# Kernel tuning notes

Hardware: AMD Instinct MI355X
Metric: run time of the kernel (lower is better)

Reference implementation:

```python
import jax, jax.numpy as jnp
import numpy as np

# DeepSeek-V3 MLA attention (q_lora_rank > 0 path), sdpa attn_type (causal)
B, S, DIM = 2, 2048, 2048
NH = 16
Q_LORA = 1536
KV_LORA = 512
NOPE = 128
ROPE = 64
VH = 128
QK_HD = NOPE + ROPE  # 192
EPS = 1e-6
SCALE = QK_HD ** -0.5
ROPE_THETA = 10000.0


def _freqs(seqlen, dim, base):
    f = 1.0 / base ** (np.arange(0, dim, 2, dtype=np.float32) / dim)
    ang = np.outer(np.arange(seqlen, dtype=np.float32), f)
    return jnp.asarray(np.cos(ang)), jnp.asarray(np.sin(ang))


def rmsnorm(x, w, eps=EPS):
    var = jnp.mean(jnp.square(x), axis=-1, keepdims=True)
    return x * jax.lax.rsqrt(var + eps) * w


def apply_rope(x, cos, sin):
    # x: [b, s, h, d]; cos/sin: [s, d//2]; interleaved complex pairs (x[2i], x[2i+1])
    xr, xi = x[..., 0::2], x[..., 1::2]
    c = cos[None, :, None, :]
    s = sin[None, :, None, :]
    yr = xr * c - xi * s
    yi = xr * s + xi * c
    return jnp.stack([yr, yi], axis=-1).reshape(x.shape)


def setup_inputs() -> dict:
    key = jax.random.key(0)
    ks = jax.random.split(key, 7)
    std = 0.02
    x = jax.random.normal(ks[0], (B, S, DIM), dtype=jnp.float32)
    cos, sin = _freqs(S, ROPE, ROPE_THETA)
    return {
        "x": x,
        "freqs_cos": cos,
        "freqs_sin": sin,
        "wq_a": jax.random.normal(ks[1], (DIM, Q_LORA), dtype=jnp.float32) * std,
        "q_norm_w": jnp.ones((Q_LORA,), dtype=jnp.float32),
        "wq_b": jax.random.normal(ks[2], (Q_LORA, NH * QK_HD), dtype=jnp.float32) * std,
        "wkv_a": jax.random.normal(ks[3], (DIM, KV_LORA + ROPE), dtype=jnp.float32) * std,
        "kv_norm_w": jnp.ones((KV_LORA,), dtype=jnp.float32),
        "wkv_b": jax.random.normal(ks[4], (KV_LORA, NH * (NOPE + VH)), dtype=jnp.float32) * std,
        "wo": jax.random.normal(ks[5], (NH * VH, DIM), dtype=jnp.float32) * std,
    }


def reference(x, freqs_cos, freqs_sin, wq_a, q_norm_w, wq_b, wkv_a, kv_norm_w, wkv_b, wo):
    b, s, _ = x.shape
    # low-rank Q projection: wq_a -> RMSNorm -> wq_b
    q = rmsnorm(x @ wq_a, q_norm_w) @ wq_b
    q = q.reshape(b, s, NH, QK_HD)
    q_nope, q_pe = q[..., :NOPE], q[..., NOPE:]
    q_pe = apply_rope(q_pe, freqs_cos, freqs_sin)
    q = jnp.concatenate([q_nope, q_pe], axis=-1)
    # low-rank KV: wkv_a -> split latent / rope part
    kv = x @ wkv_a
    kv_lat, k_pe = kv[..., :KV_LORA], kv[..., KV_LORA:]
    k_pe = apply_rope(k_pe[:, :, None, :], freqs_cos, freqs_sin)  # [b,s,1,ROPE]
    kv = rmsnorm(kv_lat, kv_norm_w) @ wkv_b
    kv = kv.reshape(b, s, NH, NOPE + VH)
    k_nope, v = kv[..., :NOPE], kv[..., NOPE:]
    k = jnp.concatenate([k_nope, jnp.broadcast_to(k_pe, (b, s, NH, ROPE))], axis=-1)
    # attention [b,h,s,d]
    q = q.transpose(0, 2, 1, 3)
    k = k.transpose(0, 2, 1, 3)
    v = v.transpose(0, 2, 1, 3)
    scores = jnp.einsum("bhqd,bhkd->bhqk", q, k) * SCALE
    causal = jnp.tril(jnp.ones((s, s), dtype=bool))
    scores = jnp.where(causal[None, None], scores, jnp.finfo(scores.dtype).min)
    probs = jax.nn.softmax(scores, axis=-1)
    out = jnp.einsum("bhqk,bhkd->bhqd", probs, v)
    out = out.transpose(0, 2, 1, 3).reshape(b, s, NH * VH)
    return out @ wo
```

## Files before the change

kernel.cpp:

```cpp
#include <hip/hip_runtime.h>
#include <cstdint>
#include <cstddef>

typedef __attribute__((ext_vector_type(8))) short bf16x8;
typedef __attribute__((ext_vector_type(4))) float f32x4;
typedef __attribute__((ext_vector_type(16))) float f32x16;

#define S_LEN 2048
#define SCALE2 0.10411754f

__device__ __forceinline__ ushort f2bf(float f) {
  uint32_t u = __float_as_uint(f);
  u = (u + 0x7FFFu + ((u >> 16) & 1u)) >> 16;
  return (ushort)u;
}
__device__ __forceinline__ float bf2f(ushort u) {
  return __uint_as_float(((uint32_t)u) << 16);
}

typedef __attribute__((address_space(1))) void GV;
typedef __attribute__((address_space(3))) void LV;
__device__ __forceinline__ void gload16(const void* g, void* l) {
  __builtin_amdgcn_global_load_lds((GV*)g, (LV*)l, 16, 0, 0);
}

__device__ __forceinline__ void store_out(float* p, float v) { *p = v; }
__device__ __forceinline__ void store_out(ushort* p, float v) { *p = f2bf(v); }

__global__ void k_f32_to_bf16(const float* __restrict__ in, ushort* __restrict__ out, int n4) {
  int i = blockIdx.x * blockDim.x + threadIdx.x;
  int stride = gridDim.x * blockDim.x;
  for (; i < n4; i += stride) {
    float4 v = reinterpret_cast<const float4*>(in)[i];
    ushort4 o;
    o.x = f2bf(v.x); o.y = f2bf(v.y); o.z = f2bf(v.z); o.w = f2bf(v.w);
    reinterpret_cast<ushort4*>(out)[i] = o;
  }
}

__global__ void k_transpose_f32_bf16(const float* __restrict__ in, ushort* __restrict__ out,
                                     int R, int C) {
  __shared__ float tile[32][33];
  int c0 = blockIdx.x * 32, r0 = blockIdx.y * 32;
  int tx = threadIdx.x, ty = threadIdx.y;
#pragma unroll
  for (int i = 0; i < 32; i += 8) {
    int r = r0 + ty + i, c = c0 + tx;
    if (r < R && c < C) tile[ty + i][tx] = in[(size_t)r * C + c];
  }
  __syncthreads();
#pragma unroll
  for (int i = 0; i < 32; i += 8) {
    int c = c0 + ty + i, r = r0 + tx;
    if (r < R && c < C) out[(size_t)c * R + r] = f2bf(tile[tx][ty + i]);
  }
}

template <typename OUT>
__global__ __launch_bounds__(256) void k_gemm(const ushort* __restrict__ A,
                                              const ushort* __restrict__ Bt,
                                              OUT* __restrict__ C, int K, int Nreal) {
  __shared__ ushort As[128 * 72];
  __shared__ ushort Bs[128 * 72];
  const int t = threadIdx.x, lane = t & 63, w = t >> 6;
  const int nwg = gridDim.x * gridDim.y;
  const int wg = blockIdx.y * gridDim.x + blockIdx.x;
  const int swz = (wg & 7) * (nwg >> 3) + (wg >> 3);
  const int m0 = (swz / gridDim.x) * 128, n0 = (swz % gridDim.x) * 128;
  const int wm = (w >> 1) * 64, wn = (w & 1) * 64;
  const int g = lane >> 4, q = lane & 15;
  f32x4 acc[4][4] = {};
  for (int kt = 0; kt < K; kt += 64) {
#pragma unroll
    for (int it = 0; it < 5; ++it) {
      int ii = it * 4 + w;
      if (ii < 18) {
        unsigned s = ii * 64 + lane;
        int r = s / 9, e = s - r * 9;
        int cg = e ^ ((r >> 3) & 7);
        if (cg > 7) cg = 0;
        gload16(A + (size_t)(m0 + r) * K + kt + cg * 8, (char*)As + ii * 1024);
        gload16(Bt + (size_t)(n0 + r) * K + kt + cg * 8, (char*)Bs + ii * 1024);
      }
    }
    asm volatile("s_waitcnt vmcnt(0)" ::: "memory");
    __syncthreads();
#pragma unroll
    for (int kh = 0; kh < 2; ++kh) {
      bf16x8 af[4], bfr[4];
#pragma unroll
      for (int mi = 0; mi < 4; mi++) {
        int row = wm + 16 * mi + q;
        int rx = (row >> 3) & 7;
        af[mi] = *(const bf16x8*)(As + row * 72 + (((kh * 4 + g) ^ rx) << 3));
      }
#pragma unroll
      for (int ni = 0; ni < 4; ni++) {
        int row = wn + 16 * ni + q;
        int rx = (row >> 3) & 7;
        bfr[ni] = *(const bf16x8*)(Bs + row * 72 + (((kh * 4 + g) ^ rx) << 3));
      }
#pragma unroll
      for (int mi = 0; mi < 4; mi++)
#pragma unroll
        for (int ni = 0; ni < 4; ni++)
          acc[mi][ni] = __builtin_amdgcn_mfma_f32_16x16x32_bf16(af[mi], bfr[ni], acc[mi][ni], 0, 0, 0);
    }
    __syncthreads();
  }
#pragma unroll
  for (int mi = 0; mi < 4; mi++)
#pragma unroll
    for (int ni = 0; ni < 4; ni++) {
      int col = n0 + wn + 16 * ni + q;
      if (col < Nreal) {
        int row = m0 + wm + 16 * mi + 4 * g;
#pragma unroll
        for (int r = 0; r < 4; r++)
          store_out(&C[(size_t)(row + r) * Nreal + col], acc[mi][ni][r]);
      }
    }
}

__global__ __launch_bounds__(256) void k_gemm_kv(const ushort* __restrict__ A,
                                                 const ushort* __restrict__ Bt,
                                                 ushort* __restrict__ kbuf,
                                                 ushort* __restrict__ vT, int K) {
  __shared__ ushort As[128 * 72];
  __shared__ ushort Bs[128 * 72];
  const int t = threadIdx.x, lane = t & 63, w = t >> 6;
  const int nwg = gridDim.x * gridDim.y;
  const int wg = blockIdx.y * gridDim.x + blockIdx.x;
  const int swz = (wg & 7) * (nwg >> 3) + (wg >> 3);
  const int m0 = (swz / gridDim.x) * 128, n0 = (swz % gridDim.x) * 128;
  const int wm = (w >> 1) * 64, wn = (w & 1) * 64;
  const int g = lane >> 4, q = lane & 15;
  f32x4 acc[4][4] = {};
  for (int kt = 0; kt < K; kt += 64) {
#pragma unroll
    for (int it = 0; it < 5; ++it) {
      int ii = it * 4 + w;
      if (ii < 18) {
        unsigned s = ii * 64 + lane;
        int r = s / 9, e = s - r * 9;
        int cg = e ^ ((r >> 3) & 7);
        if (cg > 7) cg = 0;
        gload16(A + (size_t)(m0 + r) * K + kt + cg * 8, (char*)As + ii * 1024);
        gload16(Bt + (size_t)(n0 + r) * K + kt + cg * 8, (char*)Bs + ii * 1024);
      }
    }
    asm volatile("s_waitcnt vmcnt(0)" ::: "memory");
    __syncthreads();
#pragma unroll
    for (int kh = 0; kh < 2; ++kh) {
      bf16x8 af[4], bfr[4];
#pragma unroll
      for (int mi = 0; mi < 4; mi++) {
        int row = wm + 16 * mi + q;
        int rx = (row >> 3) & 7;
        af[mi] = *(const bf16x8*)(As + row * 72 + (((kh * 4 + g) ^ rx) << 3));
      }
#pragma unroll
      for (int ni = 0; ni < 4; ni++) {
        int row = wn + 16 * ni + q;
        int rx = (row >> 3) & 7;
        bfr[ni] = *(const bf16x8*)(Bs + row * 72 + (((kh * 4 + g) ^ rx) << 3));
      }
#pragma unroll
      for (int mi = 0; mi < 4; mi++)
#pragma unroll
        for (int ni = 0; ni < 4; ni++)
          acc[mi][ni] = __builtin_amdgcn_mfma_f32_16x16x32_bf16(af[mi], bfr[ni], acc[mi][ni], 0, 0, 0);
    }
    __syncthreads();
  }
#pragma unroll
  for (int mi = 0; mi < 4; mi++)
#pragma unroll
    for (int ni = 0; ni < 4; ni++) {
      int col = n0 + wn + 16 * ni + q;
      int hh = col >> 8, jj = col & 255;
      int row0 = m0 + wm + 16 * mi + 4 * g;
#pragma unroll
      for (int r = 0; r < 4; r++) {
        int tok = row0 + r;
        int bb = tok >> 11, ss = tok & 2047;
        ushort v = f2bf(acc[mi][ni][r]);
        if (jj < 128)
          kbuf[((size_t)(bb * 16 + hh) * 2048 + ss) * 192 + jj] = v;
        else
          vT[((size_t)(bb * 16 + hh) * 128 + (jj - 128)) * 2048 + ss] = v;
      }
    }
}

__global__ void k_rmsnorm_bf16(const float* __restrict__ in, const float* __restrict__ w,
                               ushort* __restrict__ out, int D, int instride) {
  int row = blockIdx.x;
  const float* x = in + (size_t)row * instride;
  ushort* o = out + (size_t)row * D;
  float ss = 0.f;
  for (int i = threadIdx.x; i < D; i += 256) { float v = x[i]; ss += v * v; }
#pragma unroll
  for (int m = 1; m < 64; m <<= 1) ss += __shfl_xor(ss, m);
  __shared__ float red[4];
  if ((threadIdx.x & 63) == 0) red[threadIdx.x >> 6] = ss;
  __syncthreads();
  float tot = red[0] + red[1] + red[2] + red[3];
  float sc = rsqrtf(tot / (float)D + 1e-6f);
  for (int i = threadIdx.x; i < D; i += 256) o[i] = f2bf(x[i] * sc * w[i]);
}

__global__ void k_kvnorm_rope(const float* __restrict__ cqkv, const float* __restrict__ w,
                              const float* __restrict__ cosT, const float* __restrict__ sinT,
                              ushort* __restrict__ ckvn, ushort* __restrict__ kbuf) {
  int tok = blockIdx.x, b = tok >> 11, s = tok & 2047;
  const float* x = cqkv + (size_t)tok * 2112 + 1536;
  float ss = 0.f;
  for (int i = threadIdx.x; i < 512; i += 256) { float v = x[i]; ss += v * v; }
#pragma unroll
  for (int m = 1; m < 64; m <<= 1) ss += __shfl_xor(ss, m);
  __shared__ float red[4];
  if ((threadIdx.x & 63) == 0) red[threadIdx.x >> 6] = ss;
  __syncthreads();
  float tot = red[0] + red[1] + red[2] + red[3];
  float sc = rsqrtf(tot / 512.f + 1e-6f);
  for (int i = threadIdx.x; i < 512; i += 256) ckvn[(size_t)tok * 512 + i] = f2bf(x[i] * sc * w[i]);
  if (threadIdx.x < 32) {
    int i = threadIdx.x;
    float xr = x[512 + 2 * i], xi = x[512 + 2 * i + 1];
    float c = cosT[s * 32 + i], sn = sinT[s * 32 + i];
    uint32_t lo = f2bf(xr * c - xi * sn);
    uint32_t hi = f2bf(xr * sn + xi * c);
    uint32_t pk = lo | (hi << 16);
#pragma unroll
    for (int h = 0; h < 16; ++h)
      *(uint32_t*)(kbuf + ((size_t)(b * 16 + h) * 2048 + s) * 192 + 128 + 2 * i) = pk;
  }
}

__global__ void k_qrope(ushort* __restrict__ qb, const float* __restrict__ cosT,
                        const float* __restrict__ sinT) {
  int tok = blockIdx.x, s = tok & (S_LEN - 1);
  for (int pp = threadIdx.x; pp < 512; pp += 256) {
    int h = pp >> 5, i = pp & 31;
    ushort* base = qb + ((size_t)tok * 16 + h) * 192 + 128;
    float xr = bf2f(base[2 * i]), xi = bf2f(base[2 * i + 1]);
    float c = cosT[s * 32 + i], sn = sinT[s * 32 + i];
    base[2 * i] = f2bf(xr * c - xi * sn);
    base[2 * i + 1] = f2bf(xr * sn + xi * c);
  }
}

__global__ __launch_bounds__(256, 2) void k_attn10(const ushort* __restrict__ qb,
                                                   const ushort* __restrict__ kb,
                                                   const ushort* __restrict__ vT,
                                                   ushort* __restrict__ aout) {
  const int id = blockIdx.x;
  const int qt = 15 - (id >> 5);
  const int bh = id & 31;
  const int h = bh & 15, b = bh >> 4;

  const int t = threadIdx.x, lane = t & 63, w = t >> 6;
  const int lq = lane & 31, hi = lane >> 5;
  const int kx = (lq >> 3) & 3;

  __shared__ ushort Ks[64 * 200];
  __shared__ ushort Vs[128 * 72];

  const ushort* kh = kb + (size_t)(b * 16 + h) * (2048 * 192);
  const ushort* vh = vT + (size_t)(b * 16 + h) * (128 * 2048);

  auto stage = [&](int k0) {
#pragma unroll
    for (int it = 0; it < 7; ++it) {
      int ii = it * 4 + w;
      if (ii < 25) {
        unsigned s = ii * 64 + lane;
        int r = s / 25, e = s - r * 25;
        int cg = e ^ ((r >> 3) & 3);
        if (cg > 23) cg = 0;
        gload16(kh + (size_t)(k0 + r) * 192 + cg * 8, (char*)Ks + ii * 1024);
      }
    }
#pragma unroll
    for (int it = 0; it < 5; ++it) {
      int ii = it * 4 + w;
      if (ii < 18) {
        unsigned s = ii * 64 + lane;
        int r = s / 9, e = s - r * 9;
        int cg = e ^ ((r >> 3) & 7);
        if (cg > 7) cg = 0;
        gload16(vh + (size_t)r * 2048 + k0 + cg * 8, (char*)Vs + ii * 1024);
      }
    }
  };

  const int q0 = qt * 128;
  const int q0w = q0 + 32 * w;
  const int qg = q0w + lq;
  const int nkt = qt * 2 + 2;

  bf16x8 qf[12];
  {
    const ushort* qp = qb + ((size_t)(b * 2048 + qg) * 16 + h) * 192 + 8 * hi;
#pragma unroll
    for (int s = 0; s < 12; ++s) qf[s] = *(const bf16x8*)(qp + 16 * s);
  }

  f32x16 oacc[4];
#pragma unroll
  for (int db = 0; db < 4; ++db)
#pragma unroll
    for (int r = 0; r < 16; ++r) oacc[db][r] = 0.f;
  float m = -1e30f, l = 0.f;

  for (int kt = 0; kt < nkt; ++kt) {
    const int k0 = kt * 64;
    stage(k0);
    asm volatile("s_waitcnt vmcnt(0)" ::: "memory");
    __syncthreads();
    if (k0 <= q0w + 31) {
      f32x16 sA, sB;
#pragma unroll
      for (int r = 0; r < 16; ++r) { sA[r] = 0.f; sB[r] = 0.f; }
      __builtin_amdgcn_s_setprio(1);
#pragma unroll
      for (int s = 0; s < 12; ++s) {
        int ch = ((2 * s + hi) ^ kx) << 3;
        bf16x8 kfA = *(const bf16x8*)(Ks + lq * 200 + ch);
        bf16x8 kfB = *(const bf16x8*)(Ks + (lq + 32) * 200 + ch);
        sA = __builtin_amdgcn_mfma_f32_32x32x16_bf16(kfA, qf[s], sA, 0, 0, 0);
        sB = __builtin_amdgcn_mfma_f32_32x32x16_bf16(kfB, qf[s], sB, 0, 0, 0);
      }
      __builtin_amdgcn_s_setprio(0);
      float svA[16], svB[16];
#pragma unroll
      for (int r = 0; r < 16; ++r) { svA[r] = sA[r]; svB[r] = sB[r]; }
      if (k0 + 63 > q0w) {
#pragma unroll
        for (int r = 0; r < 16; ++r) {
          int kk = (r & 3) + 8 * (r >> 2) + 4 * hi;
          if (k0 + kk > qg) svA[r] = -1e30f;
          if (k0 + 32 + kk > qg) svB[r] = -1e30f;
        }
      }
      float pmax = fmaxf(svA[0], svB[0]);
#pragma unroll
      for (int r = 1; r < 16; ++r) pmax = fmaxf(pmax, fmaxf(svA[r], svB[r]));
      pmax = fmaxf(pmax, __shfl_xor(pmax, 32));
      float smax = pmax * SCALE2;
      if (!__all(smax - m <= 8.0f)) {
        float mnew = fmaxf(m, smax);
        float a = exp2f(m - mnew);
        l *= a;
#pragma unroll
        for (int db = 0; db < 4; ++db)
#pragma unroll
          for (int r = 0; r < 16; ++r) oacc[db][r] *= a;
        m = mnew;
      }
      float eA[16], eB[16]; float sum = 0.f;
#pragma unroll
      for (int r = 0; r < 16; ++r) {
        eA[r] = exp2f(svA[r] * SCALE2 - m);
        eB[r] = exp2f(svB[r] * SCALE2 - m);
        sum += eA[r] + eB[r];
      }
      sum += __shfl_xor(sum, 32);
      l += sum;
      uint32_t pkA[8], pkB[8];
#pragma unroll
      for (int i = 0; i < 8; ++i) {
        pkA[i] = (uint32_t)f2bf(eA[2 * i]) | ((uint32_t)f2bf(eA[2 * i + 1]) << 16);
        pkB[i] = (uint32_t)f2bf(eB[2 * i]) | ((uint32_t)f2bf(eB[2 * i + 1]) << 16);
      }
      uint32_t swA[8], swB[8];
#pragma unroll
      for (int i = 0; i < 8; ++i) {
        swA[i] = (uint32_t)__shfl_xor((int)pkA[i], 32);
        swB[i] = (uint32_t)__shfl_xor((int)pkB[i], 32);
      }
      union { uint32_t u[4]; bf16x8 v; } pA0, pA1, pB0, pB1;
      pA0.u[0] = hi ? swA[2] : pkA[0];
      pA0.u[1] = hi ? swA[3] : pkA[1];
      pA0.u[2] = hi ? pkA[2] : swA[0];
      pA0.u[3] = hi ? pkA[3] : swA[1];
      pA1.u[0] = hi ? swA[6] : pkA[4];
      pA1.u[1] = hi ? swA[7] : pkA[5];
      pA1.u[2] = hi ? pkA[6] : swA[4];
      pA1.u[3] = hi ? pkA[7] : swA[5];
      pB0.u[0] = hi ? swB[2] : pkB[0];
      pB0.u[1] = hi ? swB[3] : pkB[1];
      pB0.u[2] = hi ? pkB[2] : swB[0];
      pB0.u[3] = hi ? pkB[3] : swB[1];
      pB1.u[0] = hi ? swB[6] : pkB[4];
      pB1.u[1] = hi ? swB[7] : pkB[5];
      pB1.u[2] = hi ? pkB[6] : swB[4];
      pB1.u[3] = hi ? pkB[7] : swB[5];
      __builtin_amdgcn_s_setprio(1);
#pragma unroll
      for (int db = 0; db < 4; ++db) {
        const int d = 32 * db + lq;
        const int vx = (d >> 3) & 7;
        const ushort* vr = Vs + d * 72;
        bf16x8 vf0 = *(const bf16x8*)(vr + (((0 + hi) ^ vx) << 3));
        bf16x8 vf1 = *(const bf16x8*)(vr + (((2 + hi) ^ vx) << 3));
        bf16x8 vf2 = *(const bf16x8*)(vr + (((4 + hi) ^ vx) << 3));
        bf16x8 vf3 = *(const bf16x8*)(vr + (((6 + hi) ^ vx) << 3));
        oacc[db] = __builtin_amdgcn_mfma_f32_32x32x16_bf16(vf0, pA0.v, oacc[db], 0, 0, 0);
        oacc[db] = __builtin_amdgcn_mfma_f32_32x32x16_bf16(vf1, pA1.v, oacc[db], 0, 0, 0);
        oacc[db] = __builtin_amdgcn_mfma_f32_32x32x16_bf16(vf2, pB0.v, oacc[db], 0, 0, 0);
        oacc[db] = __builtin_amdgcn_mfma_f32_32x32x16_bf16(vf3, pB1.v, oacc[db], 0, 0, 0);
      }
      __builtin_amdgcn_s_setprio(0);
    }
    asm volatile("s_waitcnt lgkmcnt(0)" ::: "memory");
    __syncthreads();
  }

  float inv = 1.f / l;
  ushort* op = aout + ((size_t)(b * 2048 + qg)) * 2048 + h * 128 + 4 * hi;
#pragma unroll
  for (int db = 0; db < 4; ++db)
#pragma unroll
    for (int i = 0; i < 8; ++i) {
      uint32_t u = (uint32_t)f2bf(oacc[db][2 * i] * inv) |
                   ((uint32_t)f2bf(oacc[db][2 * i + 1] * inv) << 16);
      int dbase = 32 * db + (i & 1) * 2 + (i >> 1) * 8;
      *(uint32_t*)(op + dbase) = u;
    }
}

extern "C" void kernel_launch(void* const* d_in, const int* in_sizes, int n_in,
                              void* d_out, int out_size, void* d_ws, size_t ws_size,
                              hipStream_t stream) {
  const float* x = (const float*)d_in[0];
  const float* fcos = (const float*)d_in[1];
  const float* fsin = (const float*)d_in[2];
  const float* wq_a = (const float*)d_in[3];
  const float* qnw = (const float*)d_in[4];
  const float* wq_b = (const float*)d_in[5];
  const float* wkv_a = (const float*)d_in[6];
  const float* kvnw = (const float*)d_in[7];
  const float* wkv_b = (const float*)d_in[8];
  const float* wo = (const float*)d_in[9];
  float* out = (float*)d_out;

  char* ws = (char*)d_ws;
  size_t off = 0;
  auto alloc = [&](size_t bytes) -> char* {
    char* p = ws + off;
    off += (bytes + 255) & ~(size_t)255;
    return p;
  };
  ushort* xb     = (ushort*)alloc(4096ull * 2048 * 2);
  ushort* wqkv_t = (ushort*)alloc(2176ull * 2048 * 2);
  ushort* wqb_t  = (ushort*)alloc(3072ull * 1536 * 2);
  ushort* wkvb_t = (ushort*)alloc(4096ull * 512 * 2);
  ushort* wo_t   = (ushort*)alloc(2048ull * 2048 * 2);
  float*  cqkv   = (float*)alloc(4096ull * 2112 * 4);
  ushort* cqn    = (ushort*)alloc(4096ull * 1536 * 2);
  ushort* ckvn   = (ushort*)alloc(4096ull * 512 * 2);
  ushort* kbuf   = (ushort*)alloc(2ull * 16 * 2048 * 192 * 2);
  ushort* qbuf   = (ushort*)cqkv;
  ushort* aout   = xb;
  ushort* vT     = wqkv_t;

  dim3 tb(32, 8);
  k_f32_to_bf16<<<2048, 256, 0, stream>>>(x, xb, 4096 * 2048 / 4);
  k_transpose_f32_bf16<<<dim3(48, 64), tb, 0, stream>>>(wq_a, wqkv_t, 2048, 1536);
  k_transpose_f32_bf16<<<dim3(18, 64), tb, 0, stream>>>(wkv_a, wqkv_t + 1536ull * 2048, 2048, 576);
  k_transpose_f32_bf16<<<dim3(96, 48), tb, 0, stream>>>(wq_b, wqb_t, 1536, 3072);
  k_transpose_f32_bf16<<<dim3(128, 16), tb, 0, stream>>>(wkv_b, wkvb_t, 512, 4096);
  k_transpose_f32_bf16<<<dim3(64, 64), tb, 0, stream>>>(wo, wo_t, 2048, 2048);

  k_gemm<float><<<dim3(17, 32), 256, 0, stream>>>(xb, wqkv_t, cqkv, 2048, 2112);

  k_rmsnorm_bf16<<<4096, 256, 0, stream>>>(cqkv, qnw, cqn, 1536, 2112);
  k_kvnorm_rope<<<4096, 256, 0, stream>>>(cqkv, kvnw, fcos, fsin, ckvn, kbuf);

  k_gemm<ushort><<<dim3(24, 32), 256, 0, stream>>>(cqn, wqb_t, qbuf, 1536, 3072);
  k_qrope<<<4096, 256, 0, stream>>>(qbuf, fcos, fsin);

  k_gemm_kv<<<dim3(32, 32), 256, 0, stream>>>(ckvn, wkvb_t, kbuf, vT, 512);

  k_attn10<<<dim3(512), 256, 0, stream>>>(qbuf, kbuf, vT, aout);

  k_gemm<float><<<dim3(16, 32), 256, 0, stream>>>(aout, wo_t, out, 2048, 2048);
}
```

Before: 354.8 us.

## Double-buffer LDS tiles in GEMM kernels to overlap loads with MFMA

```diff
diff --git a/kernel.cpp b/kernel.cpp
--- a/kernel.cpp
+++ b/kernel.cpp
@@ -60,8 +60,8 @@
 __global__ __launch_bounds__(256) void k_gemm(const ushort* __restrict__ A,
                                               const ushort* __restrict__ Bt,
                                               OUT* __restrict__ C, int K, int Nreal) {
-  __shared__ ushort As[128 * 72];
-  __shared__ ushort Bs[128 * 72];
+  __shared__ ushort As[2][128 * 72];
+  __shared__ ushort Bs[2][128 * 72];
   const int t = threadIdx.x, lane = t & 63, w = t >> 6;
   const int nwg = gridDim.x * gridDim.y;
   const int wg = blockIdx.y * gridDim.x + blockIdx.x;
@@ -69,8 +69,9 @@
   const int m0 = (swz / gridDim.x) * 128, n0 = (swz % gridDim.x) * 128;
   const int wm = (w >> 1) * 64, wn = (w & 1) * 64;
   const int g = lane >> 4, q = lane & 15;
-  f32x4 acc[4][4] = {};
-  for (int kt = 0; kt < K; kt += 64) {
+  const int nt = K >> 6;
+
+  auto stage = [&](int kt, int p) {
 #pragma unroll
     for (int it = 0; it < 5; ++it) {
       int ii = it * 4 + w;
@@ -79,12 +80,20 @@
         int r = s / 9, e = s - r * 9;
         int cg = e ^ ((r >> 3) & 7);
         if (cg > 7) cg = 0;
-        gload16(A + (size_t)(m0 + r) * K + kt + cg * 8, (char*)As + ii * 1024);
-        gload16(Bt + (size_t)(n0 + r) * K + kt + cg * 8, (char*)Bs + ii * 1024);
-      }
-    }
-    asm volatile("s_waitcnt vmcnt(0)" ::: "memory");
-    __syncthreads();
+        gload16(A + (size_t)(m0 + r) * K + kt * 64 + cg * 8, (char*)&As[p][0] + ii * 1024);
+        gload16(Bt + (size_t)(n0 + r) * K + kt * 64 + cg * 8, (char*)&Bs[p][0] + ii * 1024);
+      }
+    }
+  };
+
+  f32x4 acc[4][4] = {};
+  stage(0, 0);
+  asm volatile("s_waitcnt vmcnt(0)" ::: "memory");
+  __syncthreads();
+
+  for (int kt = 0; kt < nt; ++kt) {
+    const int p = kt & 1;
+    if (kt + 1 < nt) stage(kt + 1, p ^ 1);
 #pragma unroll
     for (int kh = 0; kh < 2; ++kh) {
       bf16x8 af[4], bfr[4];
@@ -92,13 +101,13 @@
       for (int mi = 0; mi < 4; mi++) {
         int row = wm + 16 * mi + q;
         int rx = (row >> 3) & 7;
-        af[mi] = *(const bf16x8*)(As + row * 72 + (((kh * 4 + g) ^ rx) << 3));
+        af[mi] = *(const bf16x8*)(&As[p][0] + row * 72 + (((kh * 4 + g) ^ rx) << 3));
       }
 #pragma unroll
       for (int ni = 0; ni < 4; ni++) {
         int row = wn + 16 * ni + q;
         int rx = (row >> 3) & 7;
-        bfr[ni] = *(const bf16x8*)(Bs + row * 72 + (((kh * 4 + g) ^ rx) << 3));
+        bfr[ni] = *(const bf16x8*)(&Bs[p][0] + row * 72 + (((kh * 4 + g) ^ rx) << 3));
       }
 #pragma unroll
       for (int mi = 0; mi < 4; mi++)
@@ -106,8 +115,10 @@
         for (int ni = 0; ni < 4; ni++)
           acc[mi][ni] = __builtin_amdgcn_mfma_f32_16x16x32_bf16(af[mi], bfr[ni], acc[mi][ni], 0, 0, 0);
     }
+    asm volatile("s_waitcnt vmcnt(0) lgkmcnt(0)" ::: "memory");
     __syncthreads();
   }
+
 #pragma unroll
   for (int mi = 0; mi < 4; mi++)
 #pragma unroll
@@ -126,8 +137,8 @@
                                                  const ushort* __restrict__ Bt,
                                                  ushort* __restrict__ kbuf,
                                                  ushort* __restrict__ vT, int K) {
-  __shared__ ushort As[128 * 72];
-  __shared__ ushort Bs[128 * 72];
+  __shared__ ushort As[2][128 * 72];
+  __shared__ ushort Bs[2][128 * 72];
   const int t = threadIdx.x, lane = t & 63, w = t >> 6;
   const int nwg = gridDim.x * gridDim.y;
   const int wg = blockIdx.y * gridDim.x + blockIdx.x;
@@ -135,8 +146,9 @@
   const int m0 = (swz / gridDim.x) * 128, n0 = (swz % gridDim.x) * 128;
   const int wm = (w >> 1) * 64, wn = (w & 1) * 64;
   const int g = lane >> 4, q = lane & 15;
-  f32x4 acc[4][4] = {};
-  for (int kt = 0; kt < K; kt += 64) {
+  const int nt = K >> 6;
+
+  auto stage = [&](int kt, int p) {
 #pragma unroll
     for (int it = 0; it < 5; ++it) {
       int ii = it * 4 + w;
@@ -145,12 +157,20 @@
         int r = s / 9, e = s - r * 9;
         int cg = e ^ ((r >> 3) & 7);
         if (cg > 7) cg = 0;
-        gload16(A + (size_t)(m0 + r) * K + kt + cg * 8, (char*)As + ii * 1024);
-        gload16(Bt + (size_t)(n0 + r) * K + kt + cg * 8, (char*)Bs + ii * 1024);
-      }
-    }
-    asm volatile("s_waitcnt vmcnt(0)" ::: "memory");
-    __syncthreads();
+        gload16(A + (size_t)(m0 + r) * K + kt * 64 + cg * 8, (char*)&As[p][0] + ii * 1024);
+        gload16(Bt + (size_t)(n0 + r) * K + kt * 64 + cg * 8, (char*)&Bs[p][0] + ii * 1024);
+      }
+    }
+  };
+
+  f32x4 acc[4][4] = {};
+  stage(0, 0);
+  asm volatile("s_waitcnt vmcnt(0)" ::: "memory");
+  __syncthreads();
+
+  for (int kt = 0; kt < nt; ++kt) {
+    const int p = kt & 1;
+    if (kt + 1 < nt) stage(kt + 1, p ^ 1);
 #pragma unroll
     for (int kh = 0; kh < 2; ++kh) {
       bf16x8 af[4], bfr[4];
@@ -158,13 +178,13 @@
       for (int mi = 0; mi < 4; mi++) {
         int row = wm + 16 * mi + q;
         int rx = (row >> 3) & 7;
-        af[mi] = *(const bf16x8*)(As + row * 72 + (((kh * 4 + g) ^ rx) << 3));
+        af[mi] = *(const bf16x8*)(&As[p][0] + row * 72 + (((kh * 4 + g) ^ rx) << 3));
       }
 #pragma unroll
       for (int ni = 0; ni < 4; ni++) {
         int row = wn + 16 * ni + q;
         int rx = (row >> 3) & 7;
-        bfr[ni] = *(const bf16x8*)(Bs + row * 72 + (((kh * 4 + g) ^ rx) << 3));
+        bfr[ni] = *(const bf16x8*)(&Bs[p][0] + row * 72 + (((kh * 4 + g) ^ rx) << 3));
       }
 #pragma unroll
       for (int mi = 0; mi < 4; mi++)
@@ -172,8 +192,10 @@
         for (int ni = 0; ni < 4; ni++)
           acc[mi][ni] = __builtin_amdgcn_mfma_f32_16x16x32_bf16(af[mi], bfr[ni], acc[mi][ni], 0, 0, 0);
     }
+    asm volatile("s_waitcnt vmcnt(0) lgkmcnt(0)" ::: "memory");
     __syncthreads();
   }
+
 #pragma unroll
   for (int mi = 0; mi < 4; mi++)
 #pragma unroll
```

Result: slower. 391.2 us (+10.3%).
